# Kernel tuning notes

Measured on AMD Instinct MI355X. Metric: run time of the kernel, lower is better.

The kernel has to match this reference:

```python
import jax, jax.numpy as jnp
import numpy as np

ITERS_MAX = 10
MSE_THRESHOLD = 1e-05
CORR_THRESHOLD = 3.0
EPS = 1e-8


def setup_inputs() -> dict:
    key = jax.random.key(0)
    k1, k2 = jax.random.split(key)
    B, M = 16, 2048
    pc_src = jax.random.normal(k1, (B, 3, M), dtype=jnp.float32)
    pc_dest = jax.random.normal(k2, (B, 3, M), dtype=jnp.float32)
    mask = jnp.ones((B, M), dtype=bool)
    return {"pc_src": pc_src, "pc_dest": pc_dest, "pc_dest_is_valid_mask": mask}


def _icp(src, dest, valid):
    # src, dest: (B, 3, M); valid: (B, M) bool over dest points.
    B, _, M = src.shape
    dtype = src.dtype
    R0 = jnp.broadcast_to(jnp.eye(3, dtype=dtype), (B, 3, 3))
    t0 = jnp.zeros((B, 3), dtype=dtype)
    mse0 = jnp.zeros((B,), dtype=dtype)
    done0 = jnp.zeros((B,), dtype=bool)
    dest_sq = (dest * dest).sum(axis=1)  # (B, M)

    def body(i, carry):
        R, t, mse, done = carry
        # transform current source estimate
        p = jnp.einsum('bij,bjm->bim', R, src) + t[:, :, None]  # (B,3,M)
        # pairwise squared distances p (rows) vs dest (cols): (B, M, M)
        d2 = ((p * p).sum(axis=1)[:, :, None]
              + dest_sq[:, None, :]
              - 2.0 * jnp.einsum('bim,bin->bmn', p, dest))
        d2 = jnp.where(valid[:, None, :], d2, jnp.inf)
        nn_d2 = jnp.maximum(d2.min(axis=-1), 0.0)      # (B, M)
        nn_idx = d2.argmin(axis=-1)                    # (B, M)
        new_mse = nn_d2.mean(axis=-1)                  # (B,)
        # gather correspondences
        q = jnp.take_along_axis(dest, nn_idx[:, None, :], axis=2)  # (B,3,M)
        # reject far correspondences
        w = (jnp.sqrt(nn_d2) < CORR_THRESHOLD).astype(dtype)        # (B, M)
        wsum = w.sum(axis=-1, keepdims=True) + EPS                  # (B,1)
        mu_s = (src * w[:, None, :]).sum(axis=-1) / wsum            # (B,3)
        mu_q = (q * w[:, None, :]).sum(axis=-1) / wsum              # (B,3)
        sc = src - mu_s[:, :, None]
        qc = q - mu_q[:, :, None]
        # weighted cross-covariance, (B,3,3); Kabsch: H = sc W qc^T
        H = jnp.einsum('bim,bjm,bm->bij', sc, qc, w)
        U, S, Vt = jnp.linalg.svd(H)
        V = jnp.swapaxes(Vt, -1, -2)
        Ut = jnp.swapaxes(U, -1, -2)
        det = jnp.linalg.det(jnp.einsum('bij,bjk->bik', V, Ut))     # (B,)
        D = jnp.zeros((B, 3, 3), dtype=dtype)
        D = D.at[:, 0, 0].set(1.0).at[:, 1, 1].set(1.0).at[:, 2, 2].set(det)
        R_new = jnp.einsum('bij,bjk,bkl->bil', V, D, Ut)
        t_new = mu_q - jnp.einsum('bij,bj->bi', R_new, mu_s)
        # freeze batch items that already converged (early stopping)
        d3 = done[:, None, None]
        R_out = jnp.where(d3, R, R_new)
        t_out = jnp.where(done[:, None], t, t_new)
        mse_out = jnp.where(done, mse, new_mse)
        done_out = done | (new_mse < MSE_THRESHOLD)
        return (R_out, t_out, mse_out, done_out)

    R, t, mse, _ = jax.lax.fori_loop(0, ITERS_MAX, body, (R0, t0, mse0, done0))
    return R, t[:, :, None], mse[:, None]


def reference(pc_src, pc_dest, pc_dest_is_valid_mask):
    # R: (B,3,3), t: (B,3,1), mse: (B,1)
    return _icp(pc_src, pc_dest, pc_dest_is_valid_mask)
```

## Files before the change

### kernel.cpp

```cpp
#include <hip/hip_runtime.h>

#define B_ 16
#define M_ 2048
#define NBLK_PER_B 16
#define NW 8
#define ITERS 10
#define MSE_THR 1e-5f
#define EPS_ 1e-8f

#define CNT_STRIDE 32
#define PART_OFF 8192
#define PSTRIDE 20
#define ROWS_PER_B 32
#define PART_SZ (B_ * ROWS_PER_B * PSTRIDE)

__device__ inline void kabsch_from_sums(const float* S, float Rn[3][3], float tn[3]) {
  float wsum = S[0] + EPS_;
  float inv = 1.f / wsum;
  float msv[3] = {S[1]*inv, S[2]*inv, S[3]*inv};
  float mqv[3] = {S[4]*inv, S[5]*inv, S[6]*inv};
  float h[3][3];
  for (int i = 0; i < 3; ++i)
    for (int j = 0; j < 3; ++j)
      h[i][j] = S[7+i*3+j] - msv[i]*S[4+j] - S[1+i]*mqv[j] + S[0]*msv[i]*mqv[j];

  float g[3][3], V[3][3];
  for (int i = 0; i < 3; ++i)
    for (int j = 0; j < 3; ++j) {
      g[i][j] = h[0][i]*h[0][j] + h[1][i]*h[1][j] + h[2][i]*h[2][j];
      V[i][j] = (i == j) ? 1.f : 0.f;
    }
  const int PP[3] = {0, 0, 1}, QQ[3] = {1, 2, 2};
  for (int sweep = 0; sweep < 6; ++sweep) {
    for (int r = 0; r < 3; ++r) {
      int p = PP[r], q = QQ[r];
      float apq = g[p][q];
      if (fabsf(apq) > 1e-30f) {
        float tau = (g[q][q] - g[p][p]) / (2.f * apq);
        float tt = (tau >= 0.f ? 1.f : -1.f) / (fabsf(tau) + sqrtf(1.f + tau*tau));
        float c = 1.f / sqrtf(1.f + tt*tt);
        float s = tt * c;
        for (int k = 0; k < 3; ++k) {
          float gkp = g[k][p], gkq = g[k][q];
          g[k][p] = c*gkp - s*gkq;
          g[k][q] = s*gkp + c*gkq;
        }
        for (int k = 0; k < 3; ++k) {
          float gpk = g[p][k], gqk = g[q][k];
          g[p][k] = c*gpk - s*gqk;
          g[q][k] = s*gpk + c*gqk;
        }
        for (int k = 0; k < 3; ++k) {
          float vkp = V[k][p], vkq = V[k][q];
          V[k][p] = c*vkp - s*vkq;
          V[k][q] = s*vkp + c*vkq;
        }
      }
    }
  }
  float lam[3] = {g[0][0], g[1][1], g[2][2]};
  for (int i = 0; i < 2; ++i)
    for (int j = i+1; j < 3; ++j)
      if (lam[i] < lam[j]) {
        float tl = lam[i]; lam[i] = lam[j]; lam[j] = tl;
        for (int k = 0; k < 3; ++k) { float tv = V[k][i]; V[k][i] = V[k][j]; V[k][j] = tv; }
      }
  float U[3][3];
  for (int k = 0; k < 3; ++k) {
    float ux = h[0][0]*V[0][k] + h[0][1]*V[1][k] + h[0][2]*V[2][k];
    float uy = h[1][0]*V[0][k] + h[1][1]*V[1][k] + h[1][2]*V[2][k];
    float uz = h[2][0]*V[0][k] + h[2][1]*V[1][k] + h[2][2]*V[2][k];
    float invs = 1.f / fmaxf(sqrtf(fmaxf(lam[k], 0.f)), 1e-20f);
    U[0][k] = ux*invs; U[1][k] = uy*invs; U[2][k] = uz*invs;
  }
  float detH = h[0][0]*(h[1][1]*h[2][2] - h[1][2]*h[2][1])
             - h[0][1]*(h[1][0]*h[2][2] - h[1][2]*h[2][0])
             + h[0][2]*(h[1][0]*h[2][1] - h[1][1]*h[2][0]);
  float d3 = (detH >= 0.f) ? 1.f : -1.f;
  for (int i = 0; i < 3; ++i)
    for (int j = 0; j < 3; ++j)
      Rn[i][j] = V[i][0]*U[j][0] + V[i][1]*U[j][1] + d3*V[i][2]*U[j][2];
  for (int i = 0; i < 3; ++i)
    tn[i] = mqv[i] - (Rn[i][0]*msv[0] + Rn[i][1]*msv[1] + Rn[i][2]*msv[2]);
}

__global__ void icp_init(unsigned* __restrict__ cnt) {
  int i = blockIdx.x * blockDim.x + threadIdx.x;
  if (i < B_ * ITERS * CNT_STRIDE) cnt[i] = 0u;
}

__global__ __launch_bounds__(512, 2) void icp_fused(const float* __restrict__ src,
                                                    const float* __restrict__ dest,
                                                    float* __restrict__ ws,
                                                    float* __restrict__ out) {
  unsigned* cnt = (unsigned*)ws;
  float* partial = ws + PART_OFF;

  int blk = blockIdx.x;
  int b = blk >> 4, sub = blk & 15;
  int tid = threadIdx.x;
  int lane = tid & 63, w = tid >> 6;

  __shared__ float4 dt[M_];
  __shared__ float mval[NW][2][64];
  __shared__ int   midx[NW][2][64];
  __shared__ float Ssh[17];
  __shared__ float Rsh[13];

#pragma unroll
  for (int k = 0; k < 4; ++k) {
    int n = tid + 512*k;
    float dx = dest[(b*3+0)*M_ + n];
    float dy = dest[(b*3+1)*M_ + n];
    float dz = dest[(b*3+2)*M_ + n];
    dt[n] = make_float4(dx, dy, dz, 0.5f*(dx*dx + dy*dy + dz*dz));
  }
  float sxr[2], syr[2], szr[2];
#pragma unroll
  for (int g = 0; g < 2; ++g) {
    int m = sub*128 + g*64 + lane;
    sxr[g] = src[(b*3+0)*M_ + m];
    syr[g] = src[(b*3+1)*M_ + m];
    szr[g] = src[(b*3+2)*M_ + m];
  }
  __syncthreads();

  float Rc[3][3] = {{1.f,0.f,0.f},{0.f,1.f,0.f},{0.f,0.f,1.f}};
  float tc[3] = {0.f, 0.f, 0.f};
  float mse = 0.f;
  bool done = false;

  const int sj0 = __builtin_amdgcn_readfirstlane(w) * 256;

  for (int it = 0; it < ITERS; ++it) {
    if (!done) {
      float npx[2], npy[2], npz[2], psq[2];
#pragma unroll
      for (int g = 0; g < 2; ++g) {
        float sx = sxr[g], sy = syr[g], sz = szr[g];
        float px = fmaf(Rc[0][0], sx, fmaf(Rc[0][1], sy, fmaf(Rc[0][2], sz, tc[0])));
        float py = fmaf(Rc[1][0], sx, fmaf(Rc[1][1], sy, fmaf(Rc[1][2], sz, tc[1])));
        float pz = fmaf(Rc[2][0], sx, fmaf(Rc[2][1], sy, fmaf(Rc[2][2], sz, tc[2])));
        npx[g] = -px; npy[g] = -py; npz[g] = -pz;
        psq[g] = px*px + py*py + pz*pz;
      }

      float bv[2][4]; int bix[2][4];
#pragma unroll
      for (int g = 0; g < 2; ++g)
#pragma unroll
        for (int u = 0; u < 4; ++u) { bv[g][u] = 3.0e38f; bix[g][u] = 0; }

      for (int j = 0; j < 256; j += 4) {
        float4 d0 = dt[sj0 + j + 0];
        float4 d1 = dt[sj0 + j + 1];
        float4 d2 = dt[sj0 + j + 2];
        float4 d3 = dt[sj0 + j + 3];
#pragma unroll
        for (int g = 0; g < 2; ++g) {
          float a0 = fmaf(npz[g], d0.z, fmaf(npy[g], d0.y, fmaf(npx[g], d0.x, d0.w)));
          float a1 = fmaf(npz[g], d1.z, fmaf(npy[g], d1.y, fmaf(npx[g], d1.x, d1.w)));
          float a2 = fmaf(npz[g], d2.z, fmaf(npy[g], d2.y, fmaf(npx[g], d2.x, d2.w)));
          float a3 = fmaf(npz[g], d3.z, fmaf(npy[g], d3.y, fmaf(npx[g], d3.x, d3.w)));
          bool l0 = a0 < bv[g][0]; bv[g][0] = l0 ? a0 : bv[g][0]; bix[g][0] = l0 ? (sj0+j+0) : bix[g][0];
          bool l1 = a1 < bv[g][1]; bv[g][1] = l1 ? a1 : bv[g][1]; bix[g][1] = l1 ? (sj0+j+1) : bix[g][1];
          bool l2 = a2 < bv[g][2]; bv[g][2] = l2 ? a2 : bv[g][2]; bix[g][2] = l2 ? (sj0+j+2) : bix[g][2];
          bool l3 = a3 < bv[g][3]; bv[g][3] = l3 ? a3 : bv[g][3]; bix[g][3] = l3 ? (sj0+j+3) : bix[g][3];
        }
      }

#pragma unroll
      for (int g = 0; g < 2; ++g) {
        float v = bv[g][0]; int ix = bix[g][0];
#pragma unroll
        for (int u = 1; u < 4; ++u) {
          bool better = (bv[g][u] < v) || (bv[g][u] == v && bix[g][u] < ix);
          v = better ? bv[g][u] : v;
          ix = better ? bix[g][u] : ix;
        }
        mval[w][g][lane] = v; midx[w][g][lane] = ix;
      }
      __syncthreads();

      if (w < 2) {
        const int g = w;
        float v = mval[0][g][lane]; int ix = midx[0][g][lane];
#pragma unroll
        for (int c = 1; c < NW; ++c) {
          float v2 = mval[c][g][lane]; int i2 = midx[c][g][lane];
          bool lt = v2 < v;
          v = lt ? v2 : v;
          ix = lt ? i2 : ix;
        }
        float nn = fmaxf(fmaf(2.f, v, psq[g]), 0.f);
        float a[17];
#pragma unroll
        for (int i = 0; i < 16; ++i) a[i] = 0.f;
        a[16] = nn;
        if (nn < 9.f) {
          float4 qd = dt[ix];
          float sx = sxr[g], sy = syr[g], sz = szr[g];
          a[0] = 1.f;
          a[1] = sx; a[2] = sy; a[3] = sz;
          a[4] = qd.x; a[5] = qd.y; a[6] = qd.z;
          a[7]  = sx*qd.x; a[8]  = sx*qd.y; a[9]  = sx*qd.z;
          a[10] = sy*qd.x; a[11] = sy*qd.y; a[12] = sy*qd.z;
          a[13] = sz*qd.x; a[14] = sz*qd.y; a[15] = sz*qd.z;
        }
#pragma unroll
        for (int i = 0; i < 17; ++i) {
          float vv = a[i];
          for (int off = 32; off > 0; off >>= 1) vv += __shfl_down(vv, off);
          a[i] = vv;
        }
        if (lane == 0) {
          float* pp = partial + (it & 1) * PART_SZ
                    + (b*ROWS_PER_B + sub*2 + g) * PSTRIDE;
#pragma unroll
          for (int i = 0; i < 17; ++i)
            __hip_atomic_store(pp + i, a[i], __ATOMIC_RELAXED, __HIP_MEMORY_SCOPE_AGENT);
        }
        asm volatile("s_waitcnt vmcnt(0)" ::: "memory");
      }
      __syncthreads();

      if (tid == 0) {
        unsigned* c = cnt + (b * ITERS + it) * CNT_STRIDE;
        __hip_atomic_fetch_add(c, 1u, __ATOMIC_RELAXED, __HIP_MEMORY_SCOPE_AGENT);
        while (__hip_atomic_load(c, __ATOMIC_RELAXED, __HIP_MEMORY_SCOPE_AGENT) < (unsigned)NBLK_PER_B)
          __builtin_amdgcn_s_sleep(2);
      }
      __syncthreads();

      if (w == 0 && lane < 17) {
        float* pp = partial + (it & 1) * PART_SZ;
        float s = 0.f;
#pragma unroll
        for (int c = 0; c < ROWS_PER_B; ++c)
          s += __hip_atomic_load(pp + (b*ROWS_PER_B + c)*PSTRIDE + lane,
                                 __ATOMIC_RELAXED, __HIP_MEMORY_SCOPE_AGENT);
        Ssh[lane] = s;
      }
      __syncthreads();
      if (w == 0) {
        float S[17];
#pragma unroll
        for (int i = 0; i < 17; ++i) S[i] = Ssh[i];
        float Rn[3][3], tn[3];
        kabsch_from_sums(S, Rn, tn);
        if (lane == 0) {
          for (int i = 0; i < 3; ++i)
            for (int j = 0; j < 3; ++j) Rsh[i*3+j] = Rn[i][j];
          for (int i = 0; i < 3; ++i) Rsh[9+i] = tn[i];
          Rsh[12] = S[16] * (1.f / (float)M_);
        }
      }
      __syncthreads();
#pragma unroll
      for (int i = 0; i < 3; ++i) {
#pragma unroll
        for (int j = 0; j < 3; ++j) Rc[i][j] = Rsh[i*3+j];
        tc[i] = Rsh[9+i];
      }
      mse = Rsh[12];
      if (mse < MSE_THR) done = true;
    }
  }

  if (sub == 0 && tid == 0) {
#pragma unroll
    for (int i = 0; i < 3; ++i)
#pragma unroll
      for (int j = 0; j < 3; ++j) out[b*9 + i*3 + j] = Rc[i][j];
#pragma unroll
    for (int i = 0; i < 3; ++i) out[144 + b*3 + i] = tc[i];
    out[192 + b] = mse;
  }
}

extern "C" void kernel_launch(void* const* d_in, const int* in_sizes, int n_in,
                              void* d_out, int out_size, void* d_ws, size_t ws_size,
                              hipStream_t stream) {
  const float* src  = (const float*)d_in[0];
  const float* dest = (const float*)d_in[1];
  float* out = (float*)d_out;
  float* ws = (float*)d_ws;

  hipLaunchKernelGGL(icp_init, dim3((B_*ITERS*CNT_STRIDE + 255)/256), dim3(256), 0,
                     stream, (unsigned*)ws);

  void* args[] = { (void*)&src, (void*)&dest, (void*)&ws, (void*)&out };
  hipLaunchCooperativeKernel((void*)icp_fused, dim3(256), dim3(512), args, 0, stream);
}
```

Baseline: 304.2 us.

## Stream dest coordinates from global memory with register prefetch instead of LDS

The inner nearest-neighbour scan now reads dest x/y/z directly from global memory as wave-uniform float4 loads, double-buffered two steps ahead, instead of reading the packed float4 table from shared memory. The half squared norm is recomputed per point inside the loop rather than read precomputed. This aims to remove LDS read traffic and latency from the hot loop in favour of cached uniform (possibly scalar) loads. The cost is extra ALU work per candidate and a dependence on cache hit rates, and the LDS table is still built but no longer used here.

```diff
diff --git a/kernel.cpp b/kernel.cpp
--- a/kernel.cpp
+++ b/kernel.cpp
@@ -131,6 +131,9 @@
   bool done = false;
 
   const int sj0 = __builtin_amdgcn_readfirstlane(w) * 256;
+  const float* bx = dest + (b*3+0)*M_ + sj0;
+  const float* by = bx + M_;
+  const float* bz = by + M_;
 
   for (int it = 0; it < ITERS; ++it) {
     if (!done) {
@@ -151,22 +154,36 @@
 #pragma unroll
         for (int u = 0; u < 4; ++u) { bv[g][u] = 3.0e38f; bix[g][u] = 0; }
 
+      float4 X0 = *(const float4*)(bx + 0);
+      float4 Y0 = *(const float4*)(by + 0);
+      float4 Z0 = *(const float4*)(bz + 0);
+      float4 X1 = *(const float4*)(bx + 4);
+      float4 Y1 = *(const float4*)(by + 4);
+      float4 Z1 = *(const float4*)(bz + 4);
+
       for (int j = 0; j < 256; j += 4) {
-        float4 d0 = dt[sj0 + j + 0];
-        float4 d1 = dt[sj0 + j + 1];
-        float4 d2 = dt[sj0 + j + 2];
-        float4 d3 = dt[sj0 + j + 3];
+        int jp = j + 8; jp = (jp > 252) ? 252 : jp;
+        float4 Xn = *(const float4*)(bx + jp);
+        float4 Yn = *(const float4*)(by + jp);
+        float4 Zn = *(const float4*)(bz + jp);
+
+        float w0 = 0.5f*(X0.x*X0.x + Y0.x*Y0.x + Z0.x*Z0.x);
+        float w1 = 0.5f*(X0.y*X0.y + Y0.y*Y0.y + Z0.y*Z0.y);
+        float w2 = 0.5f*(X0.z*X0.z + Y0.z*Y0.z + Z0.z*Z0.z);
+        float w3 = 0.5f*(X0.w*X0.w + Y0.w*Y0.w + Z0.w*Z0.w);
 #pragma unroll
         for (int g = 0; g < 2; ++g) {
-          float a0 = fmaf(npz[g], d0.z, fmaf(npy[g], d0.y, fmaf(npx[g], d0.x, d0.w)));
-          float a1 = fmaf(npz[g], d1.z, fmaf(npy[g], d1.y, fmaf(npx[g], d1.x, d1.w)));
-          float a2 = fmaf(npz[g], d2.z, fmaf(npy[g], d2.y, fmaf(npx[g], d2.x, d2.w)));
-          float a3 = fmaf(npz[g], d3.z, fmaf(npy[g], d3.y, fmaf(npx[g], d3.x, d3.w)));
+          float a0 = fmaf(npz[g], Z0.x, fmaf(npy[g], Y0.x, fmaf(npx[g], X0.x, w0)));
+          float a1 = fmaf(npz[g], Z0.y, fmaf(npy[g], Y0.y, fmaf(npx[g], X0.y, w1)));
+          float a2 = fmaf(npz[g], Z0.z, fmaf(npy[g], Y0.z, fmaf(npx[g], X0.z, w2)));
+          float a3 = fmaf(npz[g], Z0.w, fmaf(npy[g], Y0.w, fmaf(npx[g], X0.w, w3)));
           bool l0 = a0 < bv[g][0]; bv[g][0] = l0 ? a0 : bv[g][0]; bix[g][0] = l0 ? (sj0+j+0) : bix[g][0];
           bool l1 = a1 < bv[g][1]; bv[g][1] = l1 ? a1 : bv[g][1]; bix[g][1] = l1 ? (sj0+j+1) : bix[g][1];
           bool l2 = a2 < bv[g][2]; bv[g][2] = l2 ? a2 : bv[g][2]; bix[g][2] = l2 ? (sj0+j+2) : bix[g][2];
           bool l3 = a3 < bv[g][3]; bv[g][3] = l3 ? a3 : bv[g][3]; bix[g][3] = l3 ? (sj0+j+3) : bix[g][3];
         }
+        X0 = X1; Y0 = Y1; Z0 = Z1;
+        X1 = Xn; Y1 = Yn; Z1 = Zn;
       }
 
 #pragma unroll
```

Result: slower. 331.7 us (+9.1%).

## Use 12 waves per block with SoA dest layout and on-the-fly norms

Applied to the files above, without the earlier changes.

Raises the block size from 512 to 768 threads (12 waves) and splits the 2048 destination points unevenly across the waves (172 or 168 each). Destination points are stored as separate X/Y/Z arrays in LDS, and the half-squared-norm is recomputed inside the inner loop instead of being stored as a fourth float4 component. The aim is more wavefronts per CU for latency hiding and a smaller LDS footprint. The cost is extra ALU work per point, three LDS loads per 4 points instead of four, and a larger cross-wave reduction.

```diff
diff --git a/kernel.cpp b/kernel.cpp
--- a/kernel.cpp
+++ b/kernel.cpp
@@ -3,7 +3,8 @@
 #define B_ 16
 #define M_ 2048
 #define NBLK_PER_B 16
-#define NW 8
+#define NW 12
+#define THREADS 768
 #define ITERS 10
 #define MSE_THR 1e-5f
 #define EPS_ 1e-8f
@@ -89,10 +90,10 @@
   if (i < B_ * ITERS * CNT_STRIDE) cnt[i] = 0u;
 }
 
-__global__ __launch_bounds__(512, 2) void icp_fused(const float* __restrict__ src,
-                                                    const float* __restrict__ dest,
-                                                    float* __restrict__ ws,
-                                                    float* __restrict__ out) {
+__global__ __launch_bounds__(THREADS, 2) void icp_fused(const float* __restrict__ src,
+                                                        const float* __restrict__ dest,
+                                                        float* __restrict__ ws,
+                                                        float* __restrict__ out) {
   unsigned* cnt = (unsigned*)ws;
   float* partial = ws + PART_OFF;
 
@@ -101,19 +102,18 @@
   int tid = threadIdx.x;
   int lane = tid & 63, w = tid >> 6;
 
-  __shared__ float4 dt[M_];
+  __shared__ __align__(16) float Xs[M_];
+  __shared__ __align__(16) float Ys[M_];
+  __shared__ __align__(16) float Zs[M_];
   __shared__ float mval[NW][2][64];
   __shared__ int   midx[NW][2][64];
   __shared__ float Ssh[17];
   __shared__ float Rsh[13];
 
-#pragma unroll
-  for (int k = 0; k < 4; ++k) {
-    int n = tid + 512*k;
-    float dx = dest[(b*3+0)*M_ + n];
-    float dy = dest[(b*3+1)*M_ + n];
-    float dz = dest[(b*3+2)*M_ + n];
-    dt[n] = make_float4(dx, dy, dz, 0.5f*(dx*dx + dy*dy + dz*dz));
+  for (int n = tid; n < M_; n += THREADS) {
+    Xs[n] = dest[(b*3+0)*M_ + n];
+    Ys[n] = dest[(b*3+1)*M_ + n];
+    Zs[n] = dest[(b*3+2)*M_ + n];
   }
   float sxr[2], syr[2], szr[2];
 #pragma unroll
@@ -130,7 +130,9 @@
   float mse = 0.f;
   bool done = false;
 
-  const int sj0 = __builtin_amdgcn_readfirstlane(w) * 256;
+  const int wu = __builtin_amdgcn_readfirstlane(w);
+  const int sj0 = (wu < 8) ? wu*172 : 1376 + (wu-8)*168;
+  const int slen = (wu < 8) ? 172 : 168;
 
   for (int it = 0; it < ITERS; ++it) {
     if (!done) {
@@ -151,17 +153,20 @@
 #pragma unroll
         for (int u = 0; u < 4; ++u) { bv[g][u] = 3.0e38f; bix[g][u] = 0; }
 
-      for (int j = 0; j < 256; j += 4) {
-        float4 d0 = dt[sj0 + j + 0];
-        float4 d1 = dt[sj0 + j + 1];
-        float4 d2 = dt[sj0 + j + 2];
-        float4 d3 = dt[sj0 + j + 3];
+      for (int j = 0; j < slen; j += 4) {
+        float4 X = *(const float4*)(&Xs[sj0 + j]);
+        float4 Y = *(const float4*)(&Ys[sj0 + j]);
+        float4 Z = *(const float4*)(&Zs[sj0 + j]);
+        float w0 = 0.5f*(X.x*X.x + Y.x*Y.x + Z.x*Z.x);
+        float w1 = 0.5f*(X.y*X.y + Y.y*Y.y + Z.y*Z.y);
+        float w2 = 0.5f*(X.z*X.z + Y.z*Y.z + Z.z*Z.z);
+        float w3 = 0.5f*(X.w*X.w + Y.w*Y.w + Z.w*Z.w);
 #pragma unroll
         for (int g = 0; g < 2; ++g) {
-          float a0 = fmaf(npz[g], d0.z, fmaf(npy[g], d0.y, fmaf(npx[g], d0.x, d0.w)));
-          float a1 = fmaf(npz[g], d1.z, fmaf(npy[g], d1.y, fmaf(npx[g], d1.x, d1.w)));
-          float a2 = fmaf(npz[g], d2.z, fmaf(npy[g], d2.y, fmaf(npx[g], d2.x, d2.w)));
-          float a3 = fmaf(npz[g], d3.z, fmaf(npy[g], d3.y, fmaf(npx[g], d3.x, d3.w)));
+          float a0 = fmaf(npz[g], Z.x, fmaf(npy[g], Y.x, fmaf(npx[g], X.x, w0)));
+          float a1 = fmaf(npz[g], Z.y, fmaf(npy[g], Y.y, fmaf(npx[g], X.y, w1)));
+          float a2 = fmaf(npz[g], Z.z, fmaf(npy[g], Y.z, fmaf(npx[g], X.z, w2)));
+          float a3 = fmaf(npz[g], Z.w, fmaf(npy[g], Y.w, fmaf(npx[g], X.w, w3)));
           bool l0 = a0 < bv[g][0]; bv[g][0] = l0 ? a0 : bv[g][0]; bix[g][0] = l0 ? (sj0+j+0) : bix[g][0];
           bool l1 = a1 < bv[g][1]; bv[g][1] = l1 ? a1 : bv[g][1]; bix[g][1] = l1 ? (sj0+j+1) : bix[g][1];
           bool l2 = a2 < bv[g][2]; bv[g][2] = l2 ? a2 : bv[g][2]; bix[g][2] = l2 ? (sj0+j+2) : bix[g][2];
@@ -198,14 +203,14 @@
         for (int i = 0; i < 16; ++i) a[i] = 0.f;
         a[16] = nn;
         if (nn < 9.f) {
-          float4 qd = dt[ix];
+          float qx = Xs[ix], qy = Ys[ix], qz = Zs[ix];
           float sx = sxr[g], sy = syr[g], sz = szr[g];
           a[0] = 1.f;
           a[1] = sx; a[2] = sy; a[3] = sz;
-          a[4] = qd.x; a[5] = qd.y; a[6] = qd.z;
-          a[7]  = sx*qd.x; a[8]  = sx*qd.y; a[9]  = sx*qd.z;
-          a[10] = sy*qd.x; a[11] = sy*qd.y; a[12] = sy*qd.z;
-          a[13] = sz*qd.x; a[14] = sz*qd.y; a[15] = sz*qd.z;
+          a[4] = qx; a[5] = qy; a[6] = qz;
+          a[7]  = sx*qx; a[8]  = sx*qy; a[9]  = sx*qz;
+          a[10] = sy*qx; a[11] = sy*qy; a[12] = sy*qz;
+          a[13] = sz*qx; a[14] = sz*qy; a[15] = sz*qz;
         }
 #pragma unroll
         for (int i = 0; i < 17; ++i) {
@@ -290,5 +295,5 @@
                      stream, (unsigned*)ws);
 
   void* args[] = { (void*)&src, (void*)&dest, (void*)&ws, (void*)&out };
-  hipLaunchCooperativeKernel((void*)icp_fused, dim3(256), dim3(512), args, 0, stream);
-}
+  hipLaunchCooperativeKernel((void*)icp_fused, dim3(256), dim3(THREADS), args, 0, stream);
+}
```

New measurement: 312.1 us. 2.6% more time.

## Pack NN search into float2 FMAs, software-pipeline LDS loads, trim barrier chain

Applied to the files above, without the earlier changes.

The inner nearest-neighbour loop now handles both source points per lane with 2-wide vector FMAs, which can map to packed FP32 instructions. It also double-buffers the LDS reads of destination points in two register banks of eight. The cross-block rendezvous changes: each of the two reducing waves signals the counter itself, so the target becomes 32 arrivals, and wave 0 spins, reads the partials and broadcasts them by shuffle. This removes two __syncthreads and the shared-memory staging of the sums. Register pressure rises with the prefetch buffers, and correctness now depends on the per-wave arrival count.

```diff
diff --git a/kernel.cpp b/kernel.cpp
--- a/kernel.cpp
+++ b/kernel.cpp
@@ -13,6 +13,9 @@
 #define PSTRIDE 20
 #define ROWS_PER_B 32
 #define PART_SZ (B_ * ROWS_PER_B * PSTRIDE)
+#define ARRIVALS (2 * NBLK_PER_B)
+
+typedef float f2 __attribute__((ext_vector_type(2)));
 
 __device__ inline void kabsch_from_sums(const float* S, float Rn[3][3], float tn[3]) {
   float wsum = S[0] + EPS_;
@@ -104,7 +107,6 @@
   __shared__ float4 dt[M_];
   __shared__ float mval[NW][2][64];
   __shared__ int   midx[NW][2][64];
-  __shared__ float Ssh[17];
   __shared__ float Rsh[13];
 
 #pragma unroll
@@ -134,7 +136,8 @@
 
   for (int it = 0; it < ITERS; ++it) {
     if (!done) {
-      float npx[2], npy[2], npz[2], psq[2];
+      float npx[2], npy[2], npz[2];
+      float psq0, psq1;
 #pragma unroll
       for (int g = 0; g < 2; ++g) {
         float sx = sxr[g], sy = syr[g], sz = szr[g];
@@ -142,70 +145,103 @@
         float py = fmaf(Rc[1][0], sx, fmaf(Rc[1][1], sy, fmaf(Rc[1][2], sz, tc[1])));
         float pz = fmaf(Rc[2][0], sx, fmaf(Rc[2][1], sy, fmaf(Rc[2][2], sz, tc[2])));
         npx[g] = -px; npy[g] = -py; npz[g] = -pz;
-        psq[g] = px*px + py*py + pz*pz;
-      }
-
-      float bv[2][4]; int bix[2][4];
-#pragma unroll
-      for (int g = 0; g < 2; ++g)
-#pragma unroll
-        for (int u = 0; u < 4; ++u) { bv[g][u] = 3.0e38f; bix[g][u] = 0; }
-
-      for (int j = 0; j < 256; j += 4) {
-        float4 d0 = dt[sj0 + j + 0];
-        float4 d1 = dt[sj0 + j + 1];
-        float4 d2 = dt[sj0 + j + 2];
-        float4 d3 = dt[sj0 + j + 3];
-#pragma unroll
-        for (int g = 0; g < 2; ++g) {
-          float a0 = fmaf(npz[g], d0.z, fmaf(npy[g], d0.y, fmaf(npx[g], d0.x, d0.w)));
-          float a1 = fmaf(npz[g], d1.z, fmaf(npy[g], d1.y, fmaf(npx[g], d1.x, d1.w)));
-          float a2 = fmaf(npz[g], d2.z, fmaf(npy[g], d2.y, fmaf(npx[g], d2.x, d2.w)));
-          float a3 = fmaf(npz[g], d3.z, fmaf(npy[g], d3.y, fmaf(npx[g], d3.x, d3.w)));
-          bool l0 = a0 < bv[g][0]; bv[g][0] = l0 ? a0 : bv[g][0]; bix[g][0] = l0 ? (sj0+j+0) : bix[g][0];
-          bool l1 = a1 < bv[g][1]; bv[g][1] = l1 ? a1 : bv[g][1]; bix[g][1] = l1 ? (sj0+j+1) : bix[g][1];
-          bool l2 = a2 < bv[g][2]; bv[g][2] = l2 ? a2 : bv[g][2]; bix[g][2] = l2 ? (sj0+j+2) : bix[g][2];
-          bool l3 = a3 < bv[g][3]; bv[g][3] = l3 ? a3 : bv[g][3]; bix[g][3] = l3 ? (sj0+j+3) : bix[g][3];
-        }
-      }
-
-#pragma unroll
-      for (int g = 0; g < 2; ++g) {
-        float v = bv[g][0]; int ix = bix[g][0];
+        float pq = px*px + py*py + pz*pz;
+        if (g == 0) psq0 = pq; else psq1 = pq;
+      }
+      f2 npx2 = {npx[0], npx[1]};
+      f2 npy2 = {npy[0], npy[1]};
+      f2 npz2 = {npz[0], npz[1]};
+
+      float bv0[4], bv1[4]; int bix0[4], bix1[4];
+#pragma unroll
+      for (int u = 0; u < 4; ++u) {
+        bv0[u] = 3.0e38f; bv1[u] = 3.0e38f; bix0[u] = 0; bix1[u] = 0;
+      }
+
+#define NNS(D, IDX, U) do {                                                      \
+        f2 vx = {(D).x, (D).x}, vy = {(D).y, (D).y};                             \
+        f2 vz = {(D).z, (D).z}, vw = {(D).w, (D).w};                             \
+        f2 aa = __builtin_elementwise_fma(npz2, vz,                              \
+                 __builtin_elementwise_fma(npy2, vy,                             \
+                  __builtin_elementwise_fma(npx2, vx, vw)));                     \
+        bool l0 = aa.x < bv0[U];                                                 \
+        bv0[U] = l0 ? aa.x : bv0[U]; bix0[U] = l0 ? (IDX) : bix0[U];             \
+        bool l1 = aa.y < bv1[U];                                                 \
+        bv1[U] = l1 ? aa.y : bv1[U]; bix1[U] = l1 ? (IDX) : bix1[U];             \
+      } while (0)
+
+      float4 A0=dt[sj0+0],  A1=dt[sj0+1],  A2=dt[sj0+2],  A3=dt[sj0+3];
+      float4 A4=dt[sj0+4],  A5=dt[sj0+5],  A6=dt[sj0+6],  A7=dt[sj0+7];
+      float4 B0=dt[sj0+8],  B1=dt[sj0+9],  B2=dt[sj0+10], B3=dt[sj0+11];
+      float4 B4=dt[sj0+12], B5=dt[sj0+13], B6=dt[sj0+14], B7=dt[sj0+15];
+
+      for (int j = 0; j < 256; j += 16) {
+        const int jp = (j + 16) & 255;
+        NNS(A0, sj0+j+0, 0);  NNS(A1, sj0+j+1, 1);
+        NNS(A2, sj0+j+2, 2);  NNS(A3, sj0+j+3, 3);
+        NNS(A4, sj0+j+4, 0);  NNS(A5, sj0+j+5, 1);
+        NNS(A6, sj0+j+6, 2);  NNS(A7, sj0+j+7, 3);
+        A0=dt[sj0+jp+0]; A1=dt[sj0+jp+1]; A2=dt[sj0+jp+2]; A3=dt[sj0+jp+3];
+        A4=dt[sj0+jp+4]; A5=dt[sj0+jp+5]; A6=dt[sj0+jp+6]; A7=dt[sj0+jp+7];
+        NNS(B0, sj0+j+8,  0); NNS(B1, sj0+j+9,  1);
+        NNS(B2, sj0+j+10, 2); NNS(B3, sj0+j+11, 3);
+        NNS(B4, sj0+j+12, 0); NNS(B5, sj0+j+13, 1);
+        NNS(B6, sj0+j+14, 2); NNS(B7, sj0+j+15, 3);
+        B0=dt[sj0+jp+8];  B1=dt[sj0+jp+9];  B2=dt[sj0+jp+10]; B3=dt[sj0+jp+11];
+        B4=dt[sj0+jp+12]; B5=dt[sj0+jp+13]; B6=dt[sj0+jp+14]; B7=dt[sj0+jp+15];
+      }
+#undef NNS
+
+      {
+        float v = bv0[0]; int ix = bix0[0];
 #pragma unroll
         for (int u = 1; u < 4; ++u) {
-          bool better = (bv[g][u] < v) || (bv[g][u] == v && bix[g][u] < ix);
-          v = better ? bv[g][u] : v;
-          ix = better ? bix[g][u] : ix;
-        }
-        mval[w][g][lane] = v; midx[w][g][lane] = ix;
+          bool better = (bv0[u] < v) || (bv0[u] == v && bix0[u] < ix);
+          v = better ? bv0[u] : v;
+          ix = better ? bix0[u] : ix;
+        }
+        mval[w][0][lane] = v; midx[w][0][lane] = ix;
+      }
+      {
+        float v = bv1[0]; int ix = bix1[0];
+#pragma unroll
+        for (int u = 1; u < 4; ++u) {
+          bool better = (bv1[u] < v) || (bv1[u] == v && bix1[u] < ix);
+          v = better ? bv1[u] : v;
+          ix = better ? bix1[u] : ix;
+        }
+        mval[w][1][lane] = v; midx[w][1][lane] = ix;
       }
       __syncthreads();
 
+      unsigned* cptr = cnt + (b * ITERS + it) * CNT_STRIDE;
+
       if (w < 2) {
-        const int g = w;
-        float v = mval[0][g][lane]; int ix = midx[0][g][lane];
+        float v = mval[0][w][lane]; int ix = midx[0][w][lane];
 #pragma unroll
         for (int c = 1; c < NW; ++c) {
-          float v2 = mval[c][g][lane]; int i2 = midx[c][g][lane];
+          float v2 = mval[c][w][lane]; int i2 = midx[c][w][lane];
           bool lt = v2 < v;
           v = lt ? v2 : v;
           ix = lt ? i2 : ix;
         }
-        float nn = fmaxf(fmaf(2.f, v, psq[g]), 0.f);
+        float psqg = (w == 0) ? psq0 : psq1;
+        float sxg = (w == 0) ? sxr[0] : sxr[1];
+        float syg = (w == 0) ? syr[0] : syr[1];
+        float szg = (w == 0) ? szr[0] : szr[1];
+        float nn = fmaxf(fmaf(2.f, v, psqg), 0.f);
         float a[17];
 #pragma unroll
         for (int i = 0; i < 16; ++i) a[i] = 0.f;
         a[16] = nn;
         if (nn < 9.f) {
           float4 qd = dt[ix];
-          float sx = sxr[g], sy = syr[g], sz = szr[g];
           a[0] = 1.f;
-          a[1] = sx; a[2] = sy; a[3] = sz;
+          a[1] = sxg; a[2] = syg; a[3] = szg;
           a[4] = qd.x; a[5] = qd.y; a[6] = qd.z;
-          a[7]  = sx*qd.x; a[8]  = sx*qd.y; a[9]  = sx*qd.z;
-          a[10] = sy*qd.x; a[11] = sy*qd.y; a[12] = sy*qd.z;
-          a[13] = sz*qd.x; a[14] = sz*qd.y; a[15] = sz*qd.z;
+          a[7]  = sxg*qd.x; a[8]  = sxg*qd.y; a[9]  = sxg*qd.z;
+          a[10] = syg*qd.x; a[11] = syg*qd.y; a[12] = syg*qd.z;
+          a[13] = szg*qd.x; a[14] = szg*qd.y; a[15] = szg*qd.z;
         }
 #pragma unroll
         for (int i = 0; i < 17; ++i) {
@@ -215,37 +251,33 @@
         }
         if (lane == 0) {
           float* pp = partial + (it & 1) * PART_SZ
-                    + (b*ROWS_PER_B + sub*2 + g) * PSTRIDE;
+                    + (b*ROWS_PER_B + sub*2 + w) * PSTRIDE;
 #pragma unroll
           for (int i = 0; i < 17; ++i)
             __hip_atomic_store(pp + i, a[i], __ATOMIC_RELAXED, __HIP_MEMORY_SCOPE_AGENT);
         }
         asm volatile("s_waitcnt vmcnt(0)" ::: "memory");
-      }
-      __syncthreads();
-
-      if (tid == 0) {
-        unsigned* c = cnt + (b * ITERS + it) * CNT_STRIDE;
-        __hip_atomic_fetch_add(c, 1u, __ATOMIC_RELAXED, __HIP_MEMORY_SCOPE_AGENT);
-        while (__hip_atomic_load(c, __ATOMIC_RELAXED, __HIP_MEMORY_SCOPE_AGENT) < (unsigned)NBLK_PER_B)
-          __builtin_amdgcn_s_sleep(2);
-      }
-      __syncthreads();
-
-      if (w == 0 && lane < 17) {
-        float* pp = partial + (it & 1) * PART_SZ;
+        if (lane == 0)
+          __hip_atomic_fetch_add(cptr, 1u, __ATOMIC_RELAXED, __HIP_MEMORY_SCOPE_AGENT);
+      }
+
+      if (w == 0) {
+        if (lane == 0) {
+          while (__hip_atomic_load(cptr, __ATOMIC_RELAXED, __HIP_MEMORY_SCOPE_AGENT)
+                 < (unsigned)ARRIVALS)
+            __builtin_amdgcn_s_sleep(1);
+        }
         float s = 0.f;
-#pragma unroll
-        for (int c = 0; c < ROWS_PER_B; ++c)
-          s += __hip_atomic_load(pp + (b*ROWS_PER_B + c)*PSTRIDE + lane,
-                                 __ATOMIC_RELAXED, __HIP_MEMORY_SCOPE_AGENT);
-        Ssh[lane] = s;
-      }
-      __syncthreads();
-      if (w == 0) {
+        if (lane < 17) {
+          const float* pp = partial + (it & 1) * PART_SZ;
+#pragma unroll
+          for (int c = 0; c < ROWS_PER_B; ++c)
+            s += __hip_atomic_load(pp + (b*ROWS_PER_B + c)*PSTRIDE + lane,
+                                   __ATOMIC_RELAXED, __HIP_MEMORY_SCOPE_AGENT);
+        }
         float S[17];
 #pragma unroll
-        for (int i = 0; i < 17; ++i) S[i] = Ssh[i];
+        for (int i = 0; i < 17; ++i) S[i] = __shfl(s, i);
         float Rn[3][3], tn[3];
         kabsch_from_sums(S, Rn, tn);
         if (lane == 0) {
```

Result: no change. 300.5 us (-1.2%).
